# Kernel tuning notes

Measured on AMD Instinct MI355X. Metric: run time of the kernel, lower is better.

The kernel has to match this reference:

```python
import jax, jax.numpy as jnp
import numpy as np

N_NODES = 50000
N_EDGES = 800000
N_FEAT = 128
N_HID = 128
N_CLASS = 40


def _mean_aggregate(x, src, dst, num_nodes):
    # PyG 'mean' aggregation: for each target node, mean of source-neighbor features.
    msgs = x[src]                                             # [E, D] gather
    sums = jax.ops.segment_sum(msgs, dst, num_segments=num_nodes)   # [N, D]
    ones = jnp.ones((src.shape[0],), dtype=x.dtype)
    cnt = jax.ops.segment_sum(ones, dst, num_segments=num_nodes)    # [N]
    return sums / jnp.maximum(cnt, 1.0)[:, None]


def setup_inputs() -> dict:
    key = jax.random.key(0)
    ks = jax.random.split(key, 8)
    x = jax.random.normal(ks[0], (N_NODES, N_FEAT), dtype=jnp.float32)
    edge_index = jax.random.randint(ks[1], (2, N_EDGES), 0, N_NODES, dtype=jnp.int64)
    s1 = 1.0 / np.sqrt(N_FEAT)
    s2 = 1.0 / np.sqrt(N_HID)
    return {
        "x": x,
        "edge_index": edge_index,
        # SAGEConv 1: lin_l acts on aggregated neighbors (has bias), lin_r on root (no bias)
        "Wl1": jax.random.normal(ks[2], (N_FEAT, N_HID), dtype=jnp.float32) * s1,
        "Wr1": jax.random.normal(ks[3], (N_FEAT, N_HID), dtype=jnp.float32) * s1,
        "b1": jnp.zeros((N_HID,), dtype=jnp.float32),
        # SAGEConv 2 (gc2)
        "Wl2": jax.random.normal(ks[4], (N_HID, N_CLASS), dtype=jnp.float32) * s2,
        "Wr2": jax.random.normal(ks[5], (N_HID, N_CLASS), dtype=jnp.float32) * s2,
        "b2": jnp.zeros((N_CLASS,), dtype=jnp.float32),
    }


def reference(x, edge_index, Wl1, Wr1, b1, Wl2, Wr2, b2):
    src, dst = edge_index[0], edge_index[1]
    n = x.shape[0]
    # Layer 1: SAGEConv -> relu (dropout is identity in eval mode)
    agg = _mean_aggregate(x, src, dst, n)                 # [N, F]
    h = jax.nn.relu(agg @ Wl1 + x @ Wr1 + b1)             # [N, H]
    # Layer 2: SAGEConv (logits)
    agg2 = _mean_aggregate(h, src, dst, n)                # [N, H]
    out = agg2 @ Wl2 + h @ Wr2 + b2                       # [N, C]
    return out
```

## Files before the change

### kernel.cpp

```cpp
#include <hip/hip_runtime.h>
#include <hip/hip_bf16.h>

#define N_FEAT 128
#define N_HID  128
#define N_CLASS 40

#define NP   256
#define PSZ  196
#define BCAP 4096
#define BCHUNK 4096

#define HSTRIDE 136

typedef __attribute__((ext_vector_type(8))) __bf16 bf16x8;
typedef __attribute__((ext_vector_type(4))) float f32x4;

__device__ __forceinline__ unsigned short f2bf(float f) {
    union { float f; unsigned int u; } v; v.f = f;
    unsigned int r = (v.u + 0x7FFFu + ((v.u >> 16) & 1u)) >> 16;
    return (unsigned short)r;
}
__device__ __forceinline__ float bf2f_lo(unsigned int p) {
    union { unsigned int u; float f; } v; v.u = p << 16; return v.f;
}
__device__ __forceinline__ float bf2f_hi(unsigned int p) {
    union { unsigned int u; float f; } v; v.u = p & 0xFFFF0000u; return v.f;
}

__device__ __forceinline__ void swz_body(const float* __restrict__ W,
                                         unsigned short* __restrict__ sw,
                                         int ncols, int t, int nt) {
    if (t >= nt * 4 * 64) return;
    int lane = t & 63;
    int bi = t >> 6;
    int kc = bi & 3, ct = bi >> 2;
    int n = lane & 15, q = lane >> 4;
    int col = ct * 16 + n;
    #pragma unroll
    for (int j = 0; j < 8; ++j) {
        int k = kc * 32 + q * 8 + j;
        float f = (col < ncols) ? W[(size_t)k * ncols + col] : 0.f;
        sw[(size_t)t * 8 + j] = f2bf(f);
    }
}
__device__ __forceinline__ void swzc_body(const float* __restrict__ Wl2,
                                          const float* __restrict__ Wr2,
                                          unsigned short* __restrict__ sw, int t) {
    if (t >= 5 * 4 * 64) return;
    int lane = t & 63;
    int bi = t >> 6;
    int kc = bi & 3, ct = bi >> 2;
    int n = lane & 15, q = lane >> 4;
    int col = ct * 16 + n;
    #pragma unroll
    for (int j = 0; j < 8; ++j) {
        int k = kc * 32 + q * 8 + j;
        float f = (col < N_CLASS) ? Wl2[(size_t)k * N_CLASS + col]
                                  : Wr2[(size_t)k * N_CLASS + (col - N_CLASS)];
        sw[(size_t)t * 8 + j] = f2bf(f);
    }
}

#define CVT_BLOCKS 1568
__global__ __launch_bounds__(256) void k_prep(const float* __restrict__ x,
                                              unsigned short* __restrict__ xb, int nElem,
                                              const float* __restrict__ Wl1,
                                              const float* __restrict__ Wr1,
                                              const float* __restrict__ Wl2,
                                              const float* __restrict__ Wr2,
                                              unsigned short* __restrict__ w1l,
                                              unsigned short* __restrict__ w1r,
                                              unsigned short* __restrict__ wc,
                                              int* __restrict__ ptail) {
    int b = blockIdx.x, t = threadIdx.x;
    if (b < CVT_BLOCKS) {
        for (int i = (b * 256 + t) * 4; i < nElem; i += CVT_BLOCKS * 256 * 4) {
            float4 v = *(const float4*)(x + i);
            ushort4 o;
            o.x = f2bf(v.x); o.y = f2bf(v.y); o.z = f2bf(v.z); o.w = f2bf(v.w);
            *(ushort4*)(xb + i) = o;
        }
        return;
    }
    b -= CVT_BLOCKS;
    if (b < 8) { swz_body(Wl1, w1l, N_HID, b * 256 + t, 8); return; }
    b -= 8;
    if (b < 8) { swz_body(Wr1, w1r, N_HID, b * 256 + t, 8); return; }
    b -= 8;
    if (b < 5) { swzc_body(Wl2, Wr2, wc, b * 256 + t); return; }
    ptail[t] = 0;
}

__global__ __launch_bounds__(256) void k_bin(const int* __restrict__ src,
                                             const int* __restrict__ dst,
                                             int* __restrict__ ptail,
                                             unsigned int* __restrict__ bins, int E) {
    __shared__ unsigned int stage[BCHUNK];
    __shared__ int lcnt[NP], lofs[NP], lcur[NP], gbase[NP];
    __shared__ int ws4[4];
    int t = threadIdx.x;
    int base = blockIdx.x * BCHUNK;
    int nE = min(BCHUNK, E - base);
    lcnt[t] = 0;
    __syncthreads();
    for (int i = t; i < nE; i += 256) {
        int d = dst[base + i];
        atomicAdd(&lcnt[d / PSZ], 1);
    }
    __syncthreads();
    {
        int v = lcnt[t];
        int lane = t & 63, wid = t >> 6;
        int inc = v;
        #pragma unroll
        for (int s = 1; s < 64; s <<= 1) {
            int u = __shfl_up(inc, s);
            if (lane >= s) inc += u;
        }
        if (lane == 63) ws4[wid] = inc;
        __syncthreads();
        int wb = 0;
        for (int w = 0; w < wid; ++w) wb += ws4[w];
        int exc = wb + inc - v;
        lofs[t] = exc;
        lcur[t] = exc;
        gbase[t] = atomicAdd(&ptail[t], v);
    }
    __syncthreads();
    for (int i = t; i < nE; i += 256) {
        int d = dst[base + i];
        int s = src[base + i];
        int p = d / PSZ;
        int pos = atomicAdd(&lcur[p], 1);
        stage[pos] = ((unsigned)p << 24) | ((unsigned)(d - p * PSZ) << 16) | (unsigned)s;
    }
    __syncthreads();
    for (int i = t; i < nE; i += 256) {
        unsigned int v = stage[i];
        int p = (int)(v >> 24);
        bins[(size_t)p * BCAP + gbase[p] + (i - lofs[p])] = v;
    }
}

__global__ __launch_bounds__(256) void k_build(const unsigned int* __restrict__ bins,
                                               const int* __restrict__ ptail,
                                               int* __restrict__ off,
                                               int* __restrict__ srt, int N) {
    int p = blockIdx.x;
    int t = threadIdx.x;
    __shared__ int ws4[4];
    __shared__ int sexc[NP];
    __shared__ int lc[256], lofs[256];
    {
        int v = ptail[t];
        int lane = t & 63, wid = t >> 6;
        int inc = v;
        #pragma unroll
        for (int s = 1; s < 64; s <<= 1) {
            int u = __shfl_up(inc, s);
            if (lane >= s) inc += u;
        }
        if (lane == 63) ws4[wid] = inc;
        __syncthreads();
        int wb = 0;
        for (int w = 0; w < wid; ++w) wb += ws4[w];
        sexc[t] = wb + inc - v;
        if (p == NP - 1 && t == NP - 1) off[N] = wb + inc;
    }
    lc[t] = 0;
    __syncthreads();
    int pb = sexc[p];
    int n = ptail[p];
    const unsigned int* bp = bins + (size_t)p * BCAP;
    for (int i = t; i < n; i += 256)
        atomicAdd(&lc[(int)((bp[i] >> 16) & 0xFF)], 1);
    __syncthreads();
    {
        int v = lc[t];
        int lane = t & 63, wid = t >> 6;
        int inc = v;
        #pragma unroll
        for (int s = 1; s < 64; s <<= 1) {
            int u = __shfl_up(inc, s);
            if (lane >= s) inc += u;
        }
        if (lane == 63) ws4[wid] = inc;
        __syncthreads();
        int wb = 0;
        for (int w = 0; w < wid; ++w) wb += ws4[w];
        lofs[t] = pb + wb + inc - v;
    }
    __syncthreads();
    int g = p * PSZ + t;
    if (t < PSZ && g < N) off[g] = lofs[t];
    __syncthreads();
    for (int i = t; i < n; i += 256) {
        unsigned int v = bp[i];
        int pos = atomicAdd(&lofs[(int)((v >> 16) & 0xFF)], 1);
        srt[pos] = (int)(v & 0xFFFFu);
    }
}

__global__ __launch_bounds__(256) void k_aggb4(const unsigned short* __restrict__ feat,
                                               const int* __restrict__ srt,
                                               const int* __restrict__ off,
                                               unsigned short* __restrict__ outp, int n_nodes) {
    int wave = (blockIdx.x * blockDim.x + threadIdx.x) >> 6;
    int lane = threadIdx.x & 63;
    if (wave >= n_nodes) return;
    int q = lane >> 4;
    int l = lane & 15;
    int beg = off[wave];
    int end = off[wave + 1];
    float a0 = 0.f, a1 = 0.f, a2 = 0.f, a3 = 0.f,
          a4 = 0.f, a5 = 0.f, a6 = 0.f, a7 = 0.f;
    int e = beg + q;
    #define ACCUM128(P) { \
        a0 += bf2f_lo(P.x); a1 += bf2f_hi(P.x); \
        a2 += bf2f_lo(P.y); a3 += bf2f_hi(P.y); \
        a4 += bf2f_lo(P.z); a5 += bf2f_hi(P.z); \
        a6 += bf2f_lo(P.w); a7 += bf2f_hi(P.w); }
    for (; e + 4 < end; e += 8) {
        int s0 = srt[e];
        int s1 = srt[e + 4];
        uint4 p0 = *(const uint4*)(feat + (size_t)s0 * N_FEAT + l * 8);
        uint4 p1 = *(const uint4*)(feat + (size_t)s1 * N_FEAT + l * 8);
        ACCUM128(p0)
        ACCUM128(p1)
    }
    if (e < end) {
        int s0 = srt[e];
        uint4 p0 = *(const uint4*)(feat + (size_t)s0 * N_FEAT + l * 8);
        ACCUM128(p0)
    }
    #undef ACCUM128
    #define RED(A) A += __shfl_xor(A, 16); A += __shfl_xor(A, 32);
    RED(a0) RED(a1) RED(a2) RED(a3) RED(a4) RED(a5) RED(a6) RED(a7)
    #undef RED
    if (q == 0) {
        int c = end - beg;
        float inv = 1.0f / (float)(c > 1 ? c : 1);
        uint4 o;
        o.x = ((unsigned int)f2bf(a1 * inv) << 16) | f2bf(a0 * inv);
        o.y = ((unsigned int)f2bf(a3 * inv) << 16) | f2bf(a2 * inv);
        o.z = ((unsigned int)f2bf(a5 * inv) << 16) | f2bf(a4 * inv);
        o.w = ((unsigned int)f2bf(a7 * inv) << 16) | f2bf(a6 * inv);
        *(uint4*)(outp + (size_t)wave * N_FEAT + l * 8) = o;
    }
}

__global__ __launch_bounds__(256) void k_gemm12(const unsigned short* __restrict__ aggb,
                                                const unsigned short* __restrict__ xb,
                                                const unsigned short* __restrict__ Bl,
                                                const unsigned short* __restrict__ Br,
                                                const float* __restrict__ bias1,
                                                const unsigned short* __restrict__ Bc,
                                                const float* __restrict__ bias2,
                                                unsigned short* __restrict__ p2b,
                                                float* __restrict__ r2, int n_nodes) {
    __shared__ unsigned short hlds[4][16 * HSTRIDE];
    int tid = threadIdx.x;
    int wv = tid >> 6;
    int wid = (blockIdx.x * 256 + tid) >> 6;
    int lane = tid & 63;
    int nb = wid * 16;
    if (nb >= n_nodes) return;
    int m = lane & 15, q = lane >> 4;
    size_t abase = (size_t)(nb + m) * N_FEAT + q * 8;
    bf16x8 Aa0 = *(const bf16x8*)(aggb + abase);
    bf16x8 Aa1 = *(const bf16x8*)(aggb + abase + 32);
    bf16x8 Aa2 = *(const bf16x8*)(aggb + abase + 64);
    bf16x8 Aa3 = *(const bf16x8*)(aggb + abase + 96);
    bf16x8 Ax0 = *(const bf16x8*)(xb + abase);
    bf16x8 Ax1 = *(const bf16x8*)(xb + abase + 32);
    bf16x8 Ax2 = *(const bf16x8*)(xb + abase + 64);
    bf16x8 Ax3 = *(const bf16x8*)(xb + abase + 96);
    const bf16x8* blp = (const bf16x8*)Bl + lane;
    const bf16x8* brp = (const bf16x8*)Br + lane;
    unsigned short* hl = hlds[wv];

    #pragma unroll
    for (int ct = 0; ct < 8; ++ct) {
        f32x4 acc = {0.f, 0.f, 0.f, 0.f};
        acc = __builtin_amdgcn_mfma_f32_16x16x32_bf16(Aa0, blp[(ct*4+0)*64], acc, 0,0,0);
        acc = __builtin_amdgcn_mfma_f32_16x16x32_bf16(Ax0, brp[(ct*4+0)*64], acc, 0,0,0);
        acc = __builtin_amdgcn_mfma_f32_16x16x32_bf16(Aa1, blp[(ct*4+1)*64], acc, 0,0,0);
        acc = __builtin_amdgcn_mfma_f32_16x16x32_bf16(Ax1, brp[(ct*4+1)*64], acc, 0,0,0);
        acc = __builtin_amdgcn_mfma_f32_16x16x32_bf16(Aa2, blp[(ct*4+2)*64], acc, 0,0,0);
        acc = __builtin_amdgcn_mfma_f32_16x16x32_bf16(Ax2, brp[(ct*4+2)*64], acc, 0,0,0);
        acc = __builtin_amdgcn_mfma_f32_16x16x32_bf16(Aa3, blp[(ct*4+3)*64], acc, 0,0,0);
        acc = __builtin_amdgcn_mfma_f32_16x16x32_bf16(Ax3, brp[(ct*4+3)*64], acc, 0,0,0);
        int col = ct * 16 + m;
        float bv = bias1[col];
        hl[(q*4 + 0) * HSTRIDE + col] = f2bf(fmaxf(acc.x + bv, 0.f));
        hl[(q*4 + 1) * HSTRIDE + col] = f2bf(fmaxf(acc.y + bv, 0.f));
        hl[(q*4 + 2) * HSTRIDE + col] = f2bf(fmaxf(acc.z + bv, 0.f));
        hl[(q*4 + 3) * HSTRIDE + col] = f2bf(fmaxf(acc.w + bv, 0.f));
    }
    bf16x8 H0 = *(const bf16x8*)(hl + m * HSTRIDE + q * 8);
    bf16x8 H1 = *(const bf16x8*)(hl + m * HSTRIDE + q * 8 + 32);
    bf16x8 H2 = *(const bf16x8*)(hl + m * HSTRIDE + q * 8 + 64);
    bf16x8 H3 = *(const bf16x8*)(hl + m * HSTRIDE + q * 8 + 96);
    const bf16x8* bcp = (const bf16x8*)Bc + lane;

    #pragma unroll
    for (int ct = 0; ct < 5; ++ct) {
        f32x4 acc = {0.f, 0.f, 0.f, 0.f};
        acc = __builtin_amdgcn_mfma_f32_16x16x32_bf16(H0, bcp[(ct*4+0)*64], acc, 0,0,0);
        acc = __builtin_amdgcn_mfma_f32_16x16x32_bf16(H1, bcp[(ct*4+1)*64], acc, 0,0,0);
        acc = __builtin_amdgcn_mfma_f32_16x16x32_bf16(H2, bcp[(ct*4+2)*64], acc, 0,0,0);
        acc = __builtin_amdgcn_mfma_f32_16x16x32_bf16(H3, bcp[(ct*4+3)*64], acc, 0,0,0);
        int col = ct * 16 + m;
        if (col < N_CLASS) {
            p2b[(size_t)(nb + q*4 + 0) * N_CLASS + col] = f2bf(acc.x);
            p2b[(size_t)(nb + q*4 + 1) * N_CLASS + col] = f2bf(acc.y);
            p2b[(size_t)(nb + q*4 + 2) * N_CLASS + col] = f2bf(acc.z);
            p2b[(size_t)(nb + q*4 + 3) * N_CLASS + col] = f2bf(acc.w);
        } else {
            int rc = col - N_CLASS;
            float bv = bias2[rc];
            r2[(size_t)(nb + q*4 + 0) * N_CLASS + rc] = acc.x + bv;
            r2[(size_t)(nb + q*4 + 1) * N_CLASS + rc] = acc.y + bv;
            r2[(size_t)(nb + q*4 + 2) * N_CLASS + rc] = acc.z + bv;
            r2[(size_t)(nb + q*4 + 3) * N_CLASS + rc] = acc.w + bv;
        }
    }
}

__global__ __launch_bounds__(256) void k_agg40(const unsigned short* __restrict__ p2b,
                                               const float* __restrict__ r2,
                                               const int* __restrict__ srt,
                                               const int* __restrict__ off,
                                               float* __restrict__ outp, int n_nodes) {
    int wave = (blockIdx.x * blockDim.x + threadIdx.x) >> 6;
    int lane = threadIdx.x & 63;
    if (wave >= n_nodes) return;
    int q = lane >> 4;
    int l = lane & 15;
    bool act = l < 10;
    int beg = off[wave];
    int end = off[wave + 1];
    float a0 = 0.f, a1 = 0.f, a2 = 0.f, a3 = 0.f;
    int e = beg + q;
    #define ACCUM40(P) { \
        a0 += bf2f_lo(P.x); a1 += bf2f_hi(P.x); \
        a2 += bf2f_lo(P.y); a3 += bf2f_hi(P.y); }
    for (; e + 4 < end; e += 8) {
        int s0 = srt[e];
        int s1 = srt[e + 4];
        if (act) {
            uint2 p0 = *(const uint2*)(p2b + (size_t)s0 * N_CLASS + l * 4);
            uint2 p1 = *(const uint2*)(p2b + (size_t)s1 * N_CLASS + l * 4);
            ACCUM40(p0)
            ACCUM40(p1)
        }
    }
    if (e < end && act) {
        int s0 = srt[e];
        uint2 p0 = *(const uint2*)(p2b + (size_t)s0 * N_CLASS + l * 4);
        ACCUM40(p0)
    }
    #undef ACCUM40
    #define RED(A) A += __shfl_xor(A, 16); A += __shfl_xor(A, 32);
    RED(a0) RED(a1) RED(a2) RED(a3)
    #undef RED
    if (lane < 10) {
        int c = end - beg;
        float inv = 1.0f / (float)(c > 1 ? c : 1);
        float4 rr = *(const float4*)(r2 + (size_t)wave * N_CLASS + lane * 4);
        float4 o;
        o.x = fmaf(a0, inv, rr.x);
        o.y = fmaf(a1, inv, rr.y);
        o.z = fmaf(a2, inv, rr.z);
        o.w = fmaf(a3, inv, rr.w);
        *(float4*)(outp + (size_t)wave * N_CLASS + lane * 4) = o;
    }
}

extern "C" void kernel_launch(void* const* d_in, const int* in_sizes, int n_in,
                              void* d_out, int out_size, void* d_ws, size_t ws_size,
                              hipStream_t stream) {
    const float* x   = (const float*)d_in[0];
    const int*   ei  = (const int*)d_in[1];
    const float* Wl1 = (const float*)d_in[2];
    const float* Wr1 = (const float*)d_in[3];
    const float* b1  = (const float*)d_in[4];
    const float* Wl2 = (const float*)d_in[5];
    const float* Wr2 = (const float*)d_in[6];
    const float* b2  = (const float*)d_in[7];
    float* out = (float*)d_out;

    const int N = in_sizes[0] / N_FEAT;
    const int E = in_sizes[1] / 2;
    const int* src = ei;
    const int* dst = ei + E;

    unsigned short* xb   = (unsigned short*)d_ws;
    unsigned short* aggb = xb + (size_t)N * N_FEAT;
    unsigned short* p2b  = aggb + (size_t)N * N_FEAT;
    float* r2 = (float*)(p2b + (size_t)N * N_CLASS);
    unsigned int* bins = (unsigned int*)p2b;
    unsigned short* w1l  = (unsigned short*)(r2 + (size_t)N * N_CLASS);
    unsigned short* w1r  = w1l + 16384;
    unsigned short* wc   = w1r + 16384;
    int* off = (int*)(wc + 10240);
    int* srt = off + N + 1;
    int* ptail = srt + E;

    const int TB = 256;
    int bblocks = (E + BCHUNK - 1) / BCHUNK;

    k_prep<<<CVT_BLOCKS + 8 + 8 + 5 + 1, TB, 0, stream>>>(x, xb, N * N_FEAT,
                                                          Wl1, Wr1, Wl2, Wr2,
                                                          w1l, w1r, wc, ptail);
    k_bin<<<bblocks, TB, 0, stream>>>(src, dst, ptail, bins, E);
    k_build<<<NP, TB, 0, stream>>>(bins, ptail, off, srt, N);

    int aggblocks = (N * 64 + TB - 1) / TB;
    int gblocks = ((N + 15) / 16 + 3) / 4;

    k_aggb4<<<aggblocks, TB, 0, stream>>>(xb, srt, off, aggb, N);
    k_gemm12<<<gblocks, TB, 0, stream>>>(aggb, xb, w1l, w1r, b1, wc, b2, p2b, r2, N);
    k_agg40<<<aggblocks, TB, 0, stream>>>(p2b, r2, srt, off, out, N);
}
```

Measured before the change: 188.5 us.

## Split first-layer neighbor aggregation into four feature-column tiles for cache locality

The first aggregation kernel now launches a separate block set for each of four 32-column slices of the bf16 feature table, in tile-major order, so each pass gathers a smaller working set that is more likely to stay in L2. Each lane now loads 4 bytes (two features) instead of 16, and the edge loop is unrolled to four independent gathers per lane to keep more loads in flight. The trade-off is four times as many waves, repeated reads of the offset and sorted-index arrays, and narrower 64-byte row segments per gather.

```diff
diff --git a/kernel.cpp b/kernel.cpp
--- a/kernel.cpp
+++ b/kernel.cpp
@@ -11,6 +11,8 @@
 #define BCHUNK 4096
 
 #define HSTRIDE 136
+
+#define AGG_TILES 4
 
 typedef __attribute__((ext_vector_type(8))) __bf16 bf16x8;
 typedef __attribute__((ext_vector_type(4))) float f32x4;
@@ -204,48 +206,46 @@
 __global__ __launch_bounds__(256) void k_aggb4(const unsigned short* __restrict__ feat,
                                                const int* __restrict__ srt,
                                                const int* __restrict__ off,
-                                               unsigned short* __restrict__ outp, int n_nodes) {
-    int wave = (blockIdx.x * blockDim.x + threadIdx.x) >> 6;
+                                               unsigned short* __restrict__ outp,
+                                               int n_nodes, int nodeblocks) {
+    int tile = blockIdx.x / nodeblocks;
+    int nb   = blockIdx.x % nodeblocks;
+    int node = nb * 4 + (threadIdx.x >> 6);
+    if (node >= n_nodes) return;
     int lane = threadIdx.x & 63;
-    if (wave >= n_nodes) return;
     int q = lane >> 4;
     int l = lane & 15;
-    int beg = off[wave];
-    int end = off[wave + 1];
-    float a0 = 0.f, a1 = 0.f, a2 = 0.f, a3 = 0.f,
-          a4 = 0.f, a5 = 0.f, a6 = 0.f, a7 = 0.f;
+    const unsigned short* fcol = feat + tile * 32 + l * 2;
+    int beg = off[node];
+    int end = off[node + 1];
+    float ax = 0.f, ay = 0.f;
     int e = beg + q;
-    #define ACCUM128(P) { \
-        a0 += bf2f_lo(P.x); a1 += bf2f_hi(P.x); \
-        a2 += bf2f_lo(P.y); a3 += bf2f_hi(P.y); \
-        a4 += bf2f_lo(P.z); a5 += bf2f_hi(P.z); \
-        a6 += bf2f_lo(P.w); a7 += bf2f_hi(P.w); }
-    for (; e + 4 < end; e += 8) {
+    for (; e + 12 < end; e += 16) {
         int s0 = srt[e];
         int s1 = srt[e + 4];
-        uint4 p0 = *(const uint4*)(feat + (size_t)s0 * N_FEAT + l * 8);
-        uint4 p1 = *(const uint4*)(feat + (size_t)s1 * N_FEAT + l * 8);
-        ACCUM128(p0)
-        ACCUM128(p1)
-    }
-    if (e < end) {
+        int s2 = srt[e + 8];
+        int s3 = srt[e + 12];
+        unsigned int p0 = *(const unsigned int*)(fcol + (size_t)s0 * N_FEAT);
+        unsigned int p1 = *(const unsigned int*)(fcol + (size_t)s1 * N_FEAT);
+        unsigned int p2 = *(const unsigned int*)(fcol + (size_t)s2 * N_FEAT);
+        unsigned int p3 = *(const unsigned int*)(fcol + (size_t)s3 * N_FEAT);
+        ax += bf2f_lo(p0); ay += bf2f_hi(p0);
+        ax += bf2f_lo(p1); ay += bf2f_hi(p1);
+        ax += bf2f_lo(p2); ay += bf2f_hi(p2);
+        ax += bf2f_lo(p3); ay += bf2f_hi(p3);
+    }
+    for (; e < end; e += 4) {
         int s0 = srt[e];
-        uint4 p0 = *(const uint4*)(feat + (size_t)s0 * N_FEAT + l * 8);
-        ACCUM128(p0)
-    }
-    #undef ACCUM128
-    #define RED(A) A += __shfl_xor(A, 16); A += __shfl_xor(A, 32);
-    RED(a0) RED(a1) RED(a2) RED(a3) RED(a4) RED(a5) RED(a6) RED(a7)
-    #undef RED
+        unsigned int p0 = *(const unsigned int*)(fcol + (size_t)s0 * N_FEAT);
+        ax += bf2f_lo(p0); ay += bf2f_hi(p0);
+    }
+    ax += __shfl_xor(ax, 16); ax += __shfl_xor(ax, 32);
+    ay += __shfl_xor(ay, 16); ay += __shfl_xor(ay, 32);
     if (q == 0) {
         int c = end - beg;
         float inv = 1.0f / (float)(c > 1 ? c : 1);
-        uint4 o;
-        o.x = ((unsigned int)f2bf(a1 * inv) << 16) | f2bf(a0 * inv);
-        o.y = ((unsigned int)f2bf(a3 * inv) << 16) | f2bf(a2 * inv);
-        o.z = ((unsigned int)f2bf(a5 * inv) << 16) | f2bf(a4 * inv);
-        o.w = ((unsigned int)f2bf(a7 * inv) << 16) | f2bf(a6 * inv);
-        *(uint4*)(outp + (size_t)wave * N_FEAT + l * 8) = o;
+        unsigned int o = ((unsigned int)f2bf(ay * inv) << 16) | f2bf(ax * inv);
+        *(unsigned int*)(outp + (size_t)node * N_FEAT + tile * 32 + l * 2) = o;
     }
 }
 
@@ -416,10 +416,11 @@
     k_bin<<<bblocks, TB, 0, stream>>>(src, dst, ptail, bins, E);
     k_build<<<NP, TB, 0, stream>>>(bins, ptail, off, srt, N);
 
+    int nodeblocks = (N + 3) / 4;
     int aggblocks = (N * 64 + TB - 1) / TB;
     int gblocks = ((N + 15) / 16 + 3) / 4;
 
-    k_aggb4<<<aggblocks, TB, 0, stream>>>(xb, srt, off, aggb, N);
+    k_aggb4<<<AGG_TILES * nodeblocks, TB, 0, stream>>>(xb, srt, off, aggb, N, nodeblocks);
     k_gemm12<<<gblocks, TB, 0, stream>>>(aggb, xb, w1l, w1r, b1, wc, b2, p2b, r2, N);
     k_agg40<<<aggblocks, TB, 0, stream>>>(p2b, r2, srt, off, out, N);
 }
```

After: 235.5 us. 24.9% more time.
